# Optimization experiments

Hardware: AMD Instinct MI355X
Metric: run time of the kernel (lower is better)

The kernel has to match this reference:

```python
import jax, jax.numpy as jnp
import numpy as np

DIM = 64
HID = DIM // 8  # 8, hidden width of pos_fc / attn_fc
B, N, V = 1024, 64, 8
NUM_IDS = 10


def setup_inputs() -> dict:
    key = jax.random.key(0)
    ks = jax.random.split(key, 24)
    stdv = 1.0 / np.sqrt(DIM * DIM)
    inp = {
        "q": jax.random.normal(ks[0], (B, N, DIM), jnp.float32),
        "k": jax.random.normal(ks[1], (B, N, V, DIM), jnp.float32),
        "pos": jax.random.normal(ks[2], (B, N, V, 4), jnp.float32),
        "strength": jax.random.normal(ks[3], (512,), jnp.float32),
        # learned params
        "q_tbl": jax.random.uniform(ks[4], (NUM_IDS, DIM * DIM), jnp.float32, -stdv, stdv),
        "k_tbl": jax.random.uniform(ks[5], (NUM_IDS, DIM * DIM), jnp.float32, -stdv, stdv),
        "v_tbl": jax.random.uniform(ks[6], (NUM_IDS, DIM * DIM), jnp.float32, -stdv, stdv),
        "pos_w1": jax.random.normal(ks[7], (4, HID), jnp.float32) * 0.5,
        "pos_b1": jax.random.normal(ks[8], (HID,), jnp.float32) * 0.1,
        "pos_w2": jax.random.normal(ks[9], (HID, DIM), jnp.float32) * 0.2,
        "pos_b2": jax.random.normal(ks[10], (DIM,), jnp.float32) * 0.1,
        "attn_w1": jax.random.normal(ks[11], (DIM, HID), jnp.float32) * 0.1,
        "attn_b1": jax.random.normal(ks[12], (HID,), jnp.float32) * 0.1,
        "attn_w2": jax.random.normal(ks[13], (HID, DIM), jnp.float32) * 0.2,
        "attn_b2": jax.random.normal(ks[14], (DIM,), jnp.float32) * 0.1,
        "out_w": jax.random.normal(ks[15], (DIM, DIM), jnp.float32) * 0.1,
        "out_b": jax.random.normal(ks[16], (DIM,), jnp.float32) * 0.1,
        "str_w": jax.random.normal(ks[17], (512, DIM), jnp.float32) * 0.04,
        "str_b": jax.random.normal(ks[18], (DIM,), jnp.float32) * 0.1,
        # int args
        "mask": jax.random.randint(ks[19], (B, N, V, 1), 0, 2, jnp.int32),
        "embed_id1": 3,
    }
    return inp


def reference(q, k, pos, strength, q_tbl, k_tbl, v_tbl,
              pos_w1, pos_b1, pos_w2, pos_b2,
              attn_w1, attn_b1, attn_w2, attn_b2,
              out_w, out_b, str_w, str_b, mask, embed_id1):
    s = strength @ str_w + str_b                       # [DIM]
    Wq = q_tbl[embed_id1].reshape(DIM, DIM)
    Wk = k_tbl[embed_id1].reshape(DIM, DIM)
    Wv = v_tbl[embed_id1].reshape(DIM, DIM)
    # F.linear(x, W) = x @ W.T ; note v is computed from k (as in source)
    qh = q @ Wq.T + s                                  # [B,N,DIM]
    kh = k @ Wk.T + s                                  # [B,N,V,DIM]
    vh = k @ Wv.T + s                                  # [B,N,V,DIM]
    p = jax.nn.relu(pos @ pos_w1 + pos_b1) @ pos_w2 + pos_b2   # [B,N,V,DIM]
    attn = kh - qh[:, :, None, :] + p                  # [B,N,V,DIM]
    attn = jax.nn.relu(attn @ attn_w1 + attn_b1) @ attn_w2 + attn_b2
    attn = jnp.where(mask == 0, jnp.float32(-1e9), attn)
    attn = jax.nn.softmax(attn, axis=-2)               # softmax over views V
    x = ((vh + p) * attn).sum(axis=2)                  # [B,N,DIM]
    x = x @ out_w + out_b
    return x
```

## Files before the change

kernel.cpp:

```cpp
#include <hip/hip_runtime.h>

#define TBL 4096

#define WS_SPB 0
#define WS_C0  64
#define WS_IMG 128
#define IMG_BH  0
#define IMG_BCT 4
#define IMG_BP  5
#define IMG_BW2 9
#define IMG_BV  13
#define IMG_BO  21

typedef __attribute__((ext_vector_type(8))) short bf16x8;
typedef __attribute__((ext_vector_type(4))) float f32x4;

__device__ inline int cvt2bf(float a, float b) {
    int r;
    asm("v_cvt_pk_bf16_f32 %0, %1, %2" : "=v"(r) : "v"(a), "v"(b));
    return r;
}

__device__ inline bf16x8 pack8(const float* x) {
    union { int4 i; bf16x8 b; } u;
    u.i.x = cvt2bf(x[0], x[1]);
    u.i.y = cvt2bf(x[2], x[3]);
    u.i.z = cvt2bf(x[4], x[5]);
    u.i.w = cvt2bf(x[6], x[7]);
    return u.b;
}

__device__ inline bf16x8 pack2f4(float4 a, float4 b) {
    float t[8] = {a.x, a.y, a.z, a.w, b.x, b.y, b.z, b.w};
    return pack8(t);
}

__device__ inline bf16x8 loadpack(const float* p) {
    float4 a = *(const float4*)p;
    float4 b = *(const float4*)(p + 4);
    return pack2f4(a, b);
}

__device__ inline float swz16(float x) {
    return __int_as_float(__builtin_amdgcn_ds_swizzle(__float_as_int(x), 0x401F));
}

__global__ __launch_bounds__(256) void precompute_kernel(
    const float* __restrict__ strength, const float* __restrict__ str_w,
    const float* __restrict__ str_b,
    const float* __restrict__ q_tbl, const float* __restrict__ k_tbl,
    const float* __restrict__ v_tbl, const float* __restrict__ out_w,
    const float* __restrict__ attn_w1, const float* __restrict__ attn_b1,
    const float* __restrict__ attn_w2,
    const float* __restrict__ pos_w2, const float* __restrict__ pos_b2,
    const int* __restrict__ embed_id, float* __restrict__ ws)
{
    __shared__ float red[4][64];
    __shared__ float red2[4][64][8];

    const int t    = threadIdx.x;
    const int b    = blockIdx.x;
    const int id   = embed_id[0];
    const int lane = t & 63;
    const int dp   = t >> 6;
    const int q4   = lane >> 4;
    const int col  = lane & 15;

    if (b == 0) {
        {
            const float* st = strength + dp * 128;
            const float* sw = str_w + (size_t)(dp * 128) * 64 + lane;
            float a0 = 0.f, a1 = 0.f, a2 = 0.f, a3 = 0.f;
            #pragma unroll
            for (int i = 0; i < 128; i += 4) {
                a0 += st[i]     * sw[(size_t)(i)     * 64];
                a1 += st[i + 1] * sw[(size_t)(i + 1) * 64];
                a2 += st[i + 2] * sw[(size_t)(i + 2) * 64];
                a3 += st[i + 3] * sw[(size_t)(i + 3) * 64];
            }
            red[dp][lane] = (a0 + a1) + (a2 + a3);
        }
        if (t < 8) {
            float c = attn_b1[t];
            #pragma unroll
            for (int d = 0; d < 64; ++d) c += pos_b2[d] * attn_w1[d * 8 + t];
            ws[WS_C0 + t] = c;
        }
        __syncthreads();
        if (t < 64)
            ws[WS_SPB + t] = red[0][t] + red[1][t] + red[2][t] + red[3][t]
                           + str_b[t] + pos_b2[t];
        return;
    }

    const int im = b - 1;

    if (im < 5) {
        float val[8];
        #pragma unroll
        for (int j = 0; j < 8; ++j) val[j] = 0.f;

        if (im < 4) {
            const float* tbl = (im < 2 ? k_tbl : q_tbl) + (size_t)id * TBL;
            const int kb = (im & 1) * 32 + q4 * 8;
            if (col < 8) {
                #pragma unroll
                for (int dd = 0; dd < 16; ++dd) {
                    const int d = dp * 16 + dd;
                    const float w = attn_w1[d * 8 + col];
                    const float4 t0 = *(const float4*)(tbl + d * 64 + kb);
                    const float4 t1 = *(const float4*)(tbl + d * 64 + kb + 4);
                    val[0] += t0.x * w; val[1] += t0.y * w;
                    val[2] += t0.z * w; val[3] += t0.w * w;
                    val[4] += t1.x * w; val[5] += t1.y * w;
                    val[6] += t1.z * w; val[7] += t1.w * w;
                }
            }
        } else {
            if (q4 == 0 && col < 8) {
                #pragma unroll
                for (int dd = 0; dd < 16; ++dd) {
                    const int d = dp * 16 + dd;
                    const float w = attn_w1[d * 8 + col];
                    #pragma unroll
                    for (int j = 0; j < 8; ++j) val[j] += pos_w2[j * 64 + d] * w;
                }
            }
        }
        #pragma unroll
        for (int j = 0; j < 8; ++j) red2[dp][lane][j] = val[j];
        __syncthreads();
        if (dp == 0) {
            const float sgn = (im == 2 || im == 3) ? -1.f : 1.f;
            float v2[8];
            #pragma unroll
            for (int j = 0; j < 8; ++j)
                v2[j] = sgn * (red2[0][lane][j] + red2[1][lane][j] +
                               red2[2][lane][j] + red2[3][lane][j]);
            ((bf16x8*)(ws + WS_IMG))[im * 64 + lane] = pack8(v2);
        }
        return;
    }

    if (dp == 0) {
        float val[8];
        #pragma unroll
        for (int j = 0; j < 8; ++j) val[j] = 0.f;

        if (im < 9) {
            const int tt = im - 5;
            if (q4 == 0) {
                #pragma unroll
                for (int j = 0; j < 8; ++j) val[j] = pos_w2[j * 64 + tt * 16 + col];
            }
        } else if (im < 13) {
            const int tt = im - 9;
            if (q4 == 0) {
                #pragma unroll
                for (int j = 0; j < 8; ++j) val[j] = attn_w2[j * 64 + tt * 16 + col];
            }
        } else if (im < 21) {
            const int e = im - 13, tt = e >> 1, c = e & 1;
            const float* p = v_tbl + (size_t)id * TBL +
                             (tt * 16 + col) * 64 + c * 32 + q4 * 8;
            const float4 t0 = *(const float4*)p;
            const float4 t1 = *(const float4*)(p + 4);
            val[0] = t0.x; val[1] = t0.y; val[2] = t0.z; val[3] = t0.w;
            val[4] = t1.x; val[5] = t1.y; val[6] = t1.z; val[7] = t1.w;
        } else {
            const int e = im - 21, tt = e >> 1, c = e & 1;
            #pragma unroll
            for (int j = 0; j < 8; ++j)
                val[j] = out_w[(c * 32 + q4 * 8 + j) * 64 + tt * 16 + col];
        }
        ((bf16x8*)(ws + WS_IMG))[im * 64 + lane] = pack8(val);
    }
}

__global__ __launch_bounds__(256, 3) void attn2d_main(
    const float* __restrict__ q, const float* __restrict__ k,
    const float* __restrict__ pos,
    const float* __restrict__ pos_w1, const float* __restrict__ pos_b1,
    const float* __restrict__ attn_b2, const float* __restrict__ out_b,
    const int* __restrict__ mask,
    const float* __restrict__ ws, float* __restrict__ out)
{
    __shared__ float rh_lds[4][16 * 12];
    __shared__ float x_lds[4][8 * 68];

    const int tid  = threadIdx.x;
    const int lane = tid & 63;
    const int wiv  = __builtin_amdgcn_readfirstlane(tid >> 6);
    const int q4   = lane >> 4;
    const int col  = lane & 15;

    float* rh_w = rh_lds[wiv];
    float* x_w  = x_lds[wiv];

    const int wid = blockIdx.x * 4 + wiv;
    const bf16x8* img = (const bf16x8*)(ws + WS_IMG);

    bf16x8 Bh[4];
    #pragma unroll
    for (int c = 0; c < 4; ++c) Bh[c] = img[(IMG_BH + c) * 64 + lane];
    const bf16x8 Bct = img[IMG_BCT * 64 + lane];
    bf16x8 Bv[4][2], Bp[4], Bw[4];
    #pragma unroll
    for (int t = 0; t < 4; ++t) {
        Bv[t][0] = img[(IMG_BV + t * 2) * 64 + lane];
        Bv[t][1] = img[(IMG_BV + t * 2 + 1) * 64 + lane];
        Bp[t]    = img[(IMG_BP + t) * 64 + lane];
        Bw[t]    = img[(IMG_BW2 + t) * 64 + lane];
    }

    float spb[4], b2a[4];
    #pragma unroll
    for (int t = 0; t < 4; ++t) {
        spb[t] = ws[WS_SPB + t * 16 + col];
        b2a[t] = attn_b2[t * 16 + col];
    }
    const float c0r = (col < 8) ? ws[WS_C0 + col] : 0.f;
    const int bnp = q4 >> 1;

#define LOADRAW(PAIR, RK, RQ, RP, RM) do {                                    \
        const size_t kb_ = ((size_t)(PAIR) * 16 + col) * 64 + q4 * 8;         \
        RK[0] = *(const float4*)(k + kb_);                                    \
        RK[1] = *(const float4*)(k + kb_ + 4);                                \
        RK[2] = *(const float4*)(k + kb_ + 32);                               \
        RK[3] = *(const float4*)(k + kb_ + 36);                               \
        const size_t qb_ = ((size_t)(PAIR) * 2 + (col >> 3)) * 64 + q4 * 8;   \
        RQ[0] = *(const float4*)(q + qb_);                                    \
        RQ[1] = *(const float4*)(q + qb_ + 4);                                \
        RQ[2] = *(const float4*)(q + qb_ + 32);                               \
        RQ[3] = *(const float4*)(q + qb_ + 36);                               \
        if (lane < 16)                                                        \
            RP = *(const float4*)(pos + ((size_t)(PAIR) * 16 + lane) * 4);    \
        RM = *(const int4*)(mask + (size_t)(PAIR) * 16 + q4 * 4);             \
    } while (0)

    float4 rk[4], rq[4], rp = make_float4(0.f, 0.f, 0.f, 0.f);
    int4   rm = make_int4(1, 1, 1, 1);
    LOADRAW(wid * 4, rk, rq, rp, rm);

    #pragma unroll
    for (int it = 0; it < 4; ++it) {
        const int pair = wid * 4 + it;

        bf16x8 Ak[2], Aq[2];
        Ak[0] = pack2f4(rk[0], rk[1]);
        Ak[1] = pack2f4(rk[2], rk[3]);
        Aq[0] = pack2f4(rq[0], rq[1]);
        Aq[1] = pack2f4(rq[2], rq[3]);
        const int mm[4] = {rm.x, rm.y, rm.z, rm.w};

        bf16x8 Ahp{};
        if (lane < 16) {
            float hv[8];
            #pragma unroll
            for (int g = 0; g < 8; ++g)
                hv[g] = fmaxf(pos_b1[g] + rp.x * pos_w1[g] + rp.y * pos_w1[8 + g] +
                              rp.z * pos_w1[16 + g] + rp.w * pos_w1[24 + g], 0.f);
            Ahp = pack8(hv);
        }

        float4 nk[4], nq[4], np = make_float4(0.f, 0.f, 0.f, 0.f);
        int4   nm = make_int4(1, 1, 1, 1);
        if (it < 3) LOADRAW(pair + 1, nk, nq, np, nm);

        f32x4 acch = {0.f, 0.f, 0.f, 0.f};
        acch = __builtin_amdgcn_mfma_f32_16x16x32_bf16(Ak[0], Bh[0], acch, 0, 0, 0);
        acch = __builtin_amdgcn_mfma_f32_16x16x32_bf16(Ak[1], Bh[1], acch, 0, 0, 0);
        acch = __builtin_amdgcn_mfma_f32_16x16x32_bf16(Aq[0], Bh[2], acch, 0, 0, 0);
        acch = __builtin_amdgcn_mfma_f32_16x16x32_bf16(Aq[1], Bh[3], acch, 0, 0, 0);
        acch = __builtin_amdgcn_mfma_f32_16x16x32_bf16(Ahp,   Bct,   acch, 0, 0, 0);
        if (col < 8) {
            #pragma unroll
            for (int r = 0; r < 4; ++r)
                rh_w[(q4 * 4 + r) * 12 + col] = fmaxf(acch[r] + c0r, 0.f);
        }

        bf16x8 Arh{};
        if (q4 == 0) {
            float4 a  = *(const float4*)&rh_w[col * 12];
            float4 bb = *(const float4*)&rh_w[col * 12 + 4];
            Arh = pack2f4(a, bb);
        }

        #pragma unroll
        for (int t = 0; t < 4; ++t) {
            f32x4 vh = {0.f, 0.f, 0.f, 0.f};
            vh = __builtin_amdgcn_mfma_f32_16x16x32_bf16(Ak[0], Bv[t][0], vh, 0, 0, 0);
            vh = __builtin_amdgcn_mfma_f32_16x16x32_bf16(Ak[1], Bv[t][1], vh, 0, 0, 0);
            vh = __builtin_amdgcn_mfma_f32_16x16x32_bf16(Ahp,   Bp[t],    vh, 0, 0, 0);
            f32x4 at = {0.f, 0.f, 0.f, 0.f};
            at = __builtin_amdgcn_mfma_f32_16x16x32_bf16(Arh, Bw[t], at, 0, 0, 0);

            float lg[4];
            #pragma unroll
            for (int r = 0; r < 4; ++r)
                lg[r] = (mm[r] != 0) ? (at[r] + b2a[t]) : -1e9f;

            float mx = fmaxf(fmaxf(lg[0], lg[1]), fmaxf(lg[2], lg[3]));
            mx = fmaxf(mx, swz16(mx));
            float wsum = 0.f, xp = 0.f;
            #pragma unroll
            for (int r = 0; r < 4; ++r) {
                const float wv = __expf(lg[r] - mx);
                wsum += wv;
                xp   += wv * (vh[r] + spb[t]);
            }
            wsum += swz16(wsum);
            xp   += swz16(xp);
            const float xv = xp * __builtin_amdgcn_rcpf(wsum);
            if ((q4 & 1) == 0)
                x_w[(it * 2 + bnp) * 68 + t * 16 + col] = xv;
        }

        if (it < 3) {
            #pragma unroll
            for (int c = 0; c < 4; ++c) { rk[c] = nk[c]; rq[c] = nq[c]; }
            rp = np; rm = nm;
        }
    }
#undef LOADRAW

    bf16x8 Ax[2];
    #pragma unroll
    for (int c = 0; c < 2; ++c)
        Ax[c] = loadpack(&x_w[(col & 7) * 68 + c * 32 + q4 * 8]);
    bf16x8 Bo[4][2];
    #pragma unroll
    for (int t = 0; t < 4; ++t) {
        Bo[t][0] = img[(IMG_BO + t * 2) * 64 + lane];
        Bo[t][1] = img[(IMG_BO + t * 2 + 1) * 64 + lane];
    }
    #pragma unroll
    for (int t = 0; t < 4; ++t) {
        f32x4 a = {0.f, 0.f, 0.f, 0.f};
        a = __builtin_amdgcn_mfma_f32_16x16x32_bf16(Ax[0], Bo[t][0], a, 0, 0, 0);
        a = __builtin_amdgcn_mfma_f32_16x16x32_bf16(Ax[1], Bo[t][1], a, 0, 0, 0);
        const float ob = out_b[t * 16 + col];
        #pragma unroll
        for (int r = 0; r < 4; ++r) {
            const int row = q4 * 4 + r;
            if (row < 8)
                out[((size_t)wid * 8 + row) * 64 + t * 16 + col] = a[r] + ob;
        }
    }
}

extern "C" void kernel_launch(void* const* d_in, const int* in_sizes, int n_in,
                              void* d_out, int out_size, void* d_ws, size_t ws_size,
                              hipStream_t stream) {
    const float* q        = (const float*)d_in[0];
    const float* k        = (const float*)d_in[1];
    const float* pos      = (const float*)d_in[2];
    const float* strength = (const float*)d_in[3];
    const float* q_tbl    = (const float*)d_in[4];
    const float* k_tbl    = (const float*)d_in[5];
    const float* v_tbl    = (const float*)d_in[6];
    const float* pos_w1   = (const float*)d_in[7];
    const float* pos_b1   = (const float*)d_in[8];
    const float* pos_w2   = (const float*)d_in[9];
    const float* pos_b2   = (const float*)d_in[10];
    const float* attn_w1  = (const float*)d_in[11];
    const float* attn_b1  = (const float*)d_in[12];
    const float* attn_w2  = (const float*)d_in[13];
    const float* attn_b2  = (const float*)d_in[14];
    const float* out_w    = (const float*)d_in[15];
    const float* out_b    = (const float*)d_in[16];
    const float* str_w    = (const float*)d_in[17];
    const float* str_b    = (const float*)d_in[18];
    const int*   mask     = (const int*)d_in[19];
    const int*   embed    = (const int*)d_in[20];
    float* ws  = (float*)d_ws;
    float* out = (float*)d_out;

    hipLaunchKernelGGL(precompute_kernel, dim3(30), dim3(256), 0, stream,
                       strength, str_w, str_b, q_tbl, k_tbl, v_tbl, out_w,
                       attn_w1, attn_b1, attn_w2, pos_w2, pos_b2, embed, ws);
    hipLaunchKernelGGL(attn2d_main, dim3(2048), dim3(256), 0, stream,
                       q, k, pos, pos_w1, pos_b1, attn_b2, out_b, mask, ws, out);
}
```

Before: 285.5 us.

## Stage MFMA weight fragments in LDS to cut VGPRs and raise occupancy

Moves the 16 Bv/Bp/Bw bf16 weight fragments out of per-thread registers. They are loaded once per block into shared memory and read back from LDS inside the per-view loop. The launch bound is raised from 3 to 4 waves per SIMD to use the freed VGPRs for more latency hiding. The x staging buffer is stored as bf16, so the final output MFMA reads it directly instead of packing floats. This adds LDS reads in the inner loop, a block barrier at startup, and an extra bf16 rounding step (software round-to-nearest) on x.

```diff
diff --git a/kernel.cpp b/kernel.cpp
--- a/kernel.cpp
+++ b/kernel.cpp
@@ -11,6 +11,7 @@
 #define IMG_BW2 9
 #define IMG_BV  13
 #define IMG_BO  21
+#define N_IMG   29
 
 typedef __attribute__((ext_vector_type(8))) short bf16x8;
 typedef __attribute__((ext_vector_type(4))) float f32x4;
@@ -39,6 +40,16 @@
     float4 a = *(const float4*)p;
     float4 b = *(const float4*)(p + 4);
     return pack2f4(a, b);
+}
+
+__device__ inline unsigned short f2bf(float f) {
+    union { float f; unsigned u; } v; v.f = f;
+    unsigned r = v.u + 0x7fffu + ((v.u >> 16) & 1u);
+    return (unsigned short)(r >> 16);
+}
+
+__device__ inline bf16x8 asbf(int4 v) {
+    union { int4 i; bf16x8 b; } u; u.i = v; return u.b;
 }
 
 __device__ inline float swz16(float x) {
@@ -177,7 +188,7 @@
     }
 }
 
-__global__ __launch_bounds__(256, 3) void attn2d_main(
+__global__ __launch_bounds__(256, 4) void attn2d_main(
     const float* __restrict__ q, const float* __restrict__ k,
     const float* __restrict__ pos,
     const float* __restrict__ pos_w1, const float* __restrict__ pos_b1,
@@ -185,8 +196,9 @@
     const int* __restrict__ mask,
     const float* __restrict__ ws, float* __restrict__ out)
 {
+    __shared__ int4 img_lds[16 * 64];
     __shared__ float rh_lds[4][16 * 12];
-    __shared__ float x_lds[4][8 * 68];
+    __shared__ unsigned short x_lds[4][8 * 72];
 
     const int tid  = threadIdx.x;
     const int lane = tid & 63;
@@ -194,24 +206,29 @@
     const int q4   = lane >> 4;
     const int col  = lane & 15;
 
+    const int4* gimg = (const int4*)(ws + WS_IMG);
+
+    {
+        #pragma unroll
+        for (int i = 0; i < 4; ++i) {
+            const int li = (tid >> 6) + i * 4;
+            const int wi = (li < 8) ? (13 + li) : (li - 3);
+            img_lds[li * 64 + lane] = gimg[wi * 64 + lane];
+        }
+    }
+    __syncthreads();
+
+#define LDIMG(IDX) asbf(img_lds[(IDX) * 64 + lane])
+
     float* rh_w = rh_lds[wiv];
-    float* x_w  = x_lds[wiv];
+    unsigned short* x_w = x_lds[wiv];
 
     const int wid = blockIdx.x * 4 + wiv;
-    const bf16x8* img = (const bf16x8*)(ws + WS_IMG);
 
     bf16x8 Bh[4];
     #pragma unroll
-    for (int c = 0; c < 4; ++c) Bh[c] = img[(IMG_BH + c) * 64 + lane];
-    const bf16x8 Bct = img[IMG_BCT * 64 + lane];
-    bf16x8 Bv[4][2], Bp[4], Bw[4];
-    #pragma unroll
-    for (int t = 0; t < 4; ++t) {
-        Bv[t][0] = img[(IMG_BV + t * 2) * 64 + lane];
-        Bv[t][1] = img[(IMG_BV + t * 2 + 1) * 64 + lane];
-        Bp[t]    = img[(IMG_BP + t) * 64 + lane];
-        Bw[t]    = img[(IMG_BW2 + t) * 64 + lane];
-    }
+    for (int c = 0; c < 4; ++c) Bh[c] = asbf(gimg[(IMG_BH + c) * 64 + lane]);
+    const bf16x8 Bct = asbf(gimg[IMG_BCT * 64 + lane]);
 
     float spb[4], b2a[4];
     #pragma unroll
@@ -288,12 +305,17 @@
 
         #pragma unroll
         for (int t = 0; t < 4; ++t) {
+            const bf16x8 Bv0 = LDIMG(t * 2);
+            const bf16x8 Bv1 = LDIMG(t * 2 + 1);
+            const bf16x8 Bp  = LDIMG(8 + t);
+            const bf16x8 Bw  = LDIMG(12 + t);
+
             f32x4 vh = {0.f, 0.f, 0.f, 0.f};
-            vh = __builtin_amdgcn_mfma_f32_16x16x32_bf16(Ak[0], Bv[t][0], vh, 0, 0, 0);
-            vh = __builtin_amdgcn_mfma_f32_16x16x32_bf16(Ak[1], Bv[t][1], vh, 0, 0, 0);
-            vh = __builtin_amdgcn_mfma_f32_16x16x32_bf16(Ahp,   Bp[t],    vh, 0, 0, 0);
+            vh = __builtin_amdgcn_mfma_f32_16x16x32_bf16(Ak[0], Bv0, vh, 0, 0, 0);
+            vh = __builtin_amdgcn_mfma_f32_16x16x32_bf16(Ak[1], Bv1, vh, 0, 0, 0);
+            vh = __builtin_amdgcn_mfma_f32_16x16x32_bf16(Ahp,   Bp,  vh, 0, 0, 0);
             f32x4 at = {0.f, 0.f, 0.f, 0.f};
-            at = __builtin_amdgcn_mfma_f32_16x16x32_bf16(Arh, Bw[t], at, 0, 0, 0);
+            at = __builtin_amdgcn_mfma_f32_16x16x32_bf16(Arh, Bw, at, 0, 0, 0);
 
             float lg[4];
             #pragma unroll
@@ -313,7 +335,7 @@
             xp   += swz16(xp);
             const float xv = xp * __builtin_amdgcn_rcpf(wsum);
             if ((q4 & 1) == 0)
-                x_w[(it * 2 + bnp) * 68 + t * 16 + col] = xv;
+                x_w[(it * 2 + bnp) * 72 + t * 16 + col] = f2bf(xv);
         }
 
         if (it < 3) {
@@ -324,16 +346,16 @@
     }
 #undef LOADRAW
 
+    bf16x8 Bo[4][2];
+    #pragma unroll
+    for (int t = 0; t < 4; ++t) {
+        Bo[t][0] = asbf(gimg[(IMG_BO + t * 2) * 64 + lane]);
+        Bo[t][1] = asbf(gimg[(IMG_BO + t * 2 + 1) * 64 + lane]);
+    }
     bf16x8 Ax[2];
     #pragma unroll
     for (int c = 0; c < 2; ++c)
-        Ax[c] = loadpack(&x_w[(col & 7) * 68 + c * 32 + q4 * 8]);
-    bf16x8 Bo[4][2];
-    #pragma unroll
-    for (int t = 0; t < 4; ++t) {
-        Bo[t][0] = img[(IMG_BO + t * 2) * 64 + lane];
-        Bo[t][1] = img[(IMG_BO + t * 2 + 1) * 64 + lane];
-    }
+        Ax[c] = *(const bf16x8*)&x_w[(col & 7) * 72 + c * 32 + q4 * 8];
     #pragma unroll
     for (int t = 0; t < 4; ++t) {
         f32x4 a = {0.f, 0.f, 0.f, 0.f};
@@ -347,6 +369,7 @@
                 out[((size_t)wid * 8 + row) * 64 + t * 16 + col] = a[r] + ob;
         }
     }
+#undef LDIMG
 }
 
 extern "C" void kernel_launch(void* const* d_in, const int* in_sizes, int n_in,
```

Result: faster. 263.8 us (-7.6%).
